# Optimization experiments

Hardware: AMD Instinct MI355X
Metric: run time of the kernel (lower is better)

Reference implementation:

```python
import jax, jax.numpy as jnp
import numpy as np

T_STEPS = 10       # T_pos = T_neg = 10 hardcoded in forward
ATTN_SCALE = 0.125 # scale hardcoded in forward (not head_dim**-0.5)
V_TH = 1.0         # spikingjelly IFNode defaults: v_threshold=1.0, v_reset=0.0 (hard reset)
SG_ALPHA = 4.0     # default Sigmoid surrogate alpha

@jax.custom_vjp
def spike(v):
    return (v >= 0.0).astype(v.dtype)

def _spike_fwd(v):
    return spike(v), v

def _spike_bwd(v, g):
    sg = jax.nn.sigmoid(SG_ALPHA * v)
    return (g * SG_ALPHA * sg * (1.0 - sg),)

spike.defvjp(_spike_fwd, _spike_bwd)

def if_node_const_input(y, T=T_STEPS):
    """Multi-step IF neuron driven by the SAME input y at every step.
    charge: v += y; fire: s = H(v - 1); hard reset: v = (1 - s) * v.
    Returns spikes of shape [T, *y.shape]."""
    def step(v, _):
        v = v + y
        s = spike(v - V_TH)
        v = (1.0 - s) * v
        return v, s
    _, spikes = jax.lax.scan(step, jnp.zeros_like(y), None, length=T)
    return spikes

def setup_inputs() -> dict:
    key = jax.random.key(0)
    ks = jax.random.split(key, 6)
    N, C = 2048, 2048
    x = jax.random.normal(ks[0], (N, C), dtype=jnp.float32)
    freqs_cis = jax.random.normal(ks[1], (N, 64), dtype=jnp.float32)  # unused by forward
    w_scale = 0.02
    wq = jax.random.normal(ks[2], (C, C), dtype=jnp.float32) * w_scale
    wk = jax.random.normal(ks[3], (C, C), dtype=jnp.float32) * w_scale
    wv = jax.random.normal(ks[4], (C, C), dtype=jnp.float32) * w_scale
    wo = jax.random.normal(ks[5], (C, C), dtype=jnp.float32) * w_scale
    return {"x": x, "freqs_cis": freqs_cis, "wq": wq, "wk": wk, "wv": wv, "wo": wo}

def reference(x, freqs_cis, wq, wk, wv, wo):
    N, C = x.shape
    n_heads, head_dim = 16, 128  # C == n_heads * head_dim; n_kv_heads == n_heads so repeat_kv is a no-op
    T = T_STEPS

    x_pos = jax.nn.relu(x)
    x_neg = jax.nn.relu(-x)

    # Input is identical at every timestep, so apply the linear once, then run IF over T.
    def branch(xb):
        q = if_node_const_input(xb @ wq)  # [T, N, C] binary spikes
        k = if_node_const_input(xb @ wk)
        v = if_node_const_input(xb @ wv)
        return q, k, v

    qp, kp, vp = branch(x_pos)
    qn, kn, vn = branch(x_neg)
    xq = (qp - qn).reshape(T, N, n_heads, head_dim)
    xk = (kp - kn).reshape(T, N, n_heads, head_dim)
    xv = (vp - vn).reshape(T, N, n_heads, head_dim)

    # no-softmax attention over the HEAD axis, per token: [T,N,H,H]
    attn = jnp.einsum('tnhd,tnmd->tnhm', xq, xk) * ATTN_SCALE
    x_attn = jnp.einsum('tnhm,tnmd->tnhd', attn, xv)          # [T,N,H,Dh]
    x_attn = jnp.swapaxes(x_attn, -1, -2).reshape(T, N, C)    # transpose(-1,-2) then merge

    xo = x_attn @ wo  # [T, N, C]
    return xo.mean(axis=0)
```

## Files before the change

kernel.cpp:

```cpp
#include <hip/hip_runtime.h>
#include <hip/hip_bf16.h>


#define LIST_CAP (512u * 1024u)
#define FLAG_EPS 4e-4f

typedef __attribute__((ext_vector_type(8))) short short8;
typedef __attribute__((ext_vector_type(16))) float floatx16;

__device__ const unsigned d_LUT[16] = {0u, 0x3FFu, 0x2AAu, 0x124u, 0x88u,
                                       0x210u, 0x20u, 0x40u, 0x80u, 0x100u,
                                       0x200u, 0u, 0u, 0u, 0u, 0u};

__device__ __forceinline__ void bf16x2_rne(float a, unsigned& p1, unsigned& p2) {
  const unsigned u = __float_as_uint(a);
  const unsigned t1 = u + 0x7FFFu + ((u >> 16) & 1u);
  p1 = t1 >> 16;
  const float r = a - __uint_as_float(t1 & 0xFFFF0000u);
  const unsigned u2 = __float_as_uint(r);
  p2 = (u2 + 0x7FFFu + ((u2 >> 16) & 1u)) >> 16;
}

template <int ZERO_CNT>
__global__ __launch_bounds__(256) void wsplit(
    const float* __restrict__ W0, const float* __restrict__ W1,
    const float* __restrict__ W2, unsigned short* __restrict__ Bpk,
    int NCT, unsigned* __restrict__ cnt) {
  if (ZERO_CNT && blockIdx.x == 0 && blockIdx.y == 0 && threadIdx.x == 0)
    *cnt = 0u;
  __shared__ float Wf[32 * 132];
  const int ct = blockIdx.x, k0 = blockIdx.y * 32;
  const int c0 = ct * 128;
  const int sel = c0 >> 11;
  const float* W = (sel == 0) ? W0 : ((sel == 1) ? W1 : W2);
  const int cc0 = c0 & 2047;
  const int t = threadIdx.x;

  const int kr = t >> 3, cq = (t & 7) * 16;
#pragma unroll
  for (int u = 0; u < 4; u++) {
    const float4 v = *(const float4*)(W + (size_t)(k0 + kr) * 2048 + cc0 + cq + 4 * u);
    *(float4*)&Wf[kr * 132 + cq + 4 * u] = v;
  }
  __syncthreads();

  const int cc = t >> 1, ch0 = (t & 1) * 2;
  unsigned short* img1 = Bpk + ((size_t)(0 * NCT + ct) * 64 + blockIdx.y) * 4096;
  unsigned short* img2 = Bpk + ((size_t)(1 * NCT + ct) * 64 + blockIdx.y) * 4096;
#pragma unroll
  for (int c = ch0; c < ch0 + 2; c++) {
    unsigned q1[8], q2[8];
#pragma unroll
    for (int e = 0; e < 8; e++) bf16x2_rne(Wf[(c * 8 + e) * 132 + cc], q1[e], q2[e]);
    const int off = cc * 32 + 8 * (c ^ ((cc >> 1) & 3));
    uint4 P1, P2;
    P1.x = q1[0] | (q1[1] << 16); P1.y = q1[2] | (q1[3] << 16);
    P1.z = q1[4] | (q1[5] << 16); P1.w = q1[6] | (q1[7] << 16);
    P2.x = q2[0] | (q2[1] << 16); P2.y = q2[2] | (q2[3] << 16);
    P2.z = q2[4] | (q2[5] << 16); P2.w = q2[6] | (q2[7] << 16);
    *(uint4*)&img1[off] = P1;
    *(uint4*)&img2[off] = P2;
  }
}

template <int RELU>
__global__ __launch_bounds__(256) void asplit(
    const float* __restrict__ src, unsigned short* __restrict__ Apk, int NRT) {
  const int rt = blockIdx.x, k0i = blockIdx.y;
  const int t = threadIdx.x;
  const int r = t >> 1, half = t & 1;
  int grow = rt * 128 + r;
  float sgn = 1.f;
  if (RELU && grow >= 2048) { grow -= 2048; sgn = -1.f; }
  const float* s = src + (size_t)grow * 2048 + k0i * 32 + half * 16;
  float f[16];
#pragma unroll
  for (int u = 0; u < 4; u++) {
    const float4 v = *(const float4*)(s + 4 * u);
    f[4 * u + 0] = v.x; f[4 * u + 1] = v.y;
    f[4 * u + 2] = v.z; f[4 * u + 3] = v.w;
  }
  if (RELU) {
#pragma unroll
    for (int e = 0; e < 16; e++) f[e] = fmaxf(sgn * f[e], 0.f);
  }
  unsigned q1[16], q2[16];
#pragma unroll
  for (int e = 0; e < 16; e++) bf16x2_rne(f[e], q1[e], q2[e]);

  unsigned short* img1 = Apk + ((size_t)(0 * NRT + rt) * 64 + k0i) * 4096;
  unsigned short* img2 = Apk + ((size_t)(1 * NRT + rt) * 64 + k0i) * 4096;
#pragma unroll
  for (int cc = 0; cc < 2; cc++) {
    const int c = half * 2 + cc;
    const int off = r * 32 + 8 * (c ^ ((r >> 1) & 3));
    const int e0 = cc * 8;
    uint4 P1, P2;
    P1.x = q1[e0 + 0] | (q1[e0 + 1] << 16); P1.y = q1[e0 + 2] | (q1[e0 + 3] << 16);
    P1.z = q1[e0 + 4] | (q1[e0 + 5] << 16); P1.w = q1[e0 + 6] | (q1[e0 + 7] << 16);
    P2.x = q2[e0 + 0] | (q2[e0 + 1] << 16); P2.y = q2[e0 + 2] | (q2[e0 + 3] << 16);
    P2.z = q2[e0 + 4] | (q2[e0 + 5] << 16); P2.w = q2[e0 + 6] | (q2[e0 + 7] << 16);
    *(uint4*)&img1[off] = P1;
    *(uint4*)&img2[off] = P2;
  }
}

template <int MODE>
__global__ __launch_bounds__(256, 4) void gemm_dma(
    const unsigned short* __restrict__ Apk, const unsigned short* __restrict__ Bpk,
    int NRT, int NCT, unsigned char* __restrict__ MaskJ,
    unsigned* __restrict__ list, unsigned* __restrict__ cnt,
    float* __restrict__ Out) {
  __shared__ unsigned short sh[4][4096];
  __shared__ unsigned lutS[16];

  const int tid = threadIdx.x;
  const int bx = blockIdx.x, by = blockIdx.y;
  const int lane = tid & 63, wave = tid >> 6;
  const int wr = wave >> 1, wc = wave & 1;
  const int lm = lane & 31, lg = lane >> 5;

  if (MODE == 0 && tid < 16) lutS[tid] = d_LUT[tid];

  const unsigned short* gsrc =
      (wave < 2) ? (Apk + ((size_t)(wave * NRT + by) * 64) * 4096)
                 : (Bpk + ((size_t)((wave - 2) * NCT + bx) * 64) * 4096);

  floatx16 acc[2][2];
#pragma unroll
  for (int i = 0; i < 2; i++)
#pragma unroll
    for (int j = 0; j < 2; j++)
#pragma unroll
      for (int e = 0; e < 16; e++) acc[i][j][e] = 0.f;

  for (int k0i = 0; k0i < 64; k0i++) {
    __syncthreads();
    const unsigned short* gp = gsrc + (size_t)k0i * 4096;
#pragma unroll
    for (int i = 0; i < 8; i++) {
      __builtin_amdgcn_global_load_lds(
          (const __attribute__((address_space(1))) unsigned*)(gp + i * 512 + lane * 8),
          (__attribute__((address_space(3))) unsigned*)(&sh[wave][i * 512]), 16, 0, 0);
    }
    __syncthreads();

#pragma unroll
    for (int ks = 0; ks < 2; ks++) {
      const int ch = ks * 2 + lg;
      short8 a1[2], a2[2], b1[2], b2[2];
#pragma unroll
      for (int it = 0; it < 2; it++) {
        const int row = 64 * wr + 32 * it + lm;
        const int off = row * 32 + 8 * (ch ^ ((row >> 1) & 3));
        a1[it] = *(const short8*)&sh[0][off];
        a2[it] = *(const short8*)&sh[1][off];
      }
#pragma unroll
      for (int jt = 0; jt < 2; jt++) {
        const int row = 64 * wc + 32 * jt + lm;
        const int off = row * 32 + 8 * (ch ^ ((row >> 1) & 3));
        b1[jt] = *(const short8*)&sh[2][off];
        b2[jt] = *(const short8*)&sh[3][off];
      }
#pragma unroll
      for (int it = 0; it < 2; it++)
#pragma unroll
        for (int jt = 0; jt < 2; jt++)
          acc[it][jt] = __builtin_amdgcn_mfma_f32_32x32x16_bf16(
              a1[it], b1[jt], acc[it][jt], 0, 0, 0);
#pragma unroll
      for (int it = 0; it < 2; it++)
#pragma unroll
        for (int jt = 0; jt < 2; jt++)
          acc[it][jt] = __builtin_amdgcn_mfma_f32_32x32x16_bf16(
              a1[it], b2[jt], acc[it][jt], 0, 0, 0);
#pragma unroll
      for (int it = 0; it < 2; it++)
#pragma unroll
        for (int jt = 0; jt < 2; jt++)
          acc[it][jt] = __builtin_amdgcn_mfma_f32_32x32x16_bf16(
              a2[it], b1[jt], acc[it][jt], 0, 0, 0);
    }
  }

#pragma unroll
  for (int it = 0; it < 2; it++) {
#pragma unroll
    for (int jt = 0; jt < 2; jt++) {
      const int gn = bx * 128 + 64 * wc + 32 * jt + lm;
#pragma unroll
      for (int reg = 0; reg < 16; reg++) {
        const int gm = by * 128 + 64 * wr + 32 * it + (reg & 3) + 8 * (reg >> 2) + 4 * lg;
        const float y = acc[it][jt][reg];
        if (MODE == 1) {
          Out[(size_t)gm * 2048 + gn] = y * 0.1f;
        } else {
          float r = __builtin_amdgcn_rcpf(y);
          r = fminf(fmaxf(r, -1.0f), 12.0f);
          const float jf = floorf(r);
          const float d0 = fmaf(jf, y, -1.0f);
          const float i0 = fminf(fmaxf(jf, 1.0f), 10.0f);
          const float i1 = fminf(fmaxf(jf + 1.0f, 1.0f), 10.0f);
          const float e0 = fmaf(i0, y, -1.0f);
          const float e1 = fmaf(i1, y, -1.0f);
          const float mind = fminf(fabsf(e0), fabsf(e1));
          const unsigned J = (unsigned)(int)((d0 >= 0.0f) ? jf : jf + 1.0f);
          MaskJ[(size_t)gm * 6144 + gn] = (unsigned char)((J <= 10u) ? J : 0u);
          if (mind < FLAG_EPS) {
            const unsigned idx = atomicAdd(cnt, 1u);
            if (idx < LIST_CAP) list[idx] = ((unsigned)gm << 13) | (unsigned)gn;
          }
        }
      }
    }
  }
}

__global__ __launch_bounds__(256) void transpose_w(
    const float* __restrict__ W0, const float* __restrict__ W1,
    const float* __restrict__ W2, float* __restrict__ WT) {
  __shared__ float tile[32][33];
  const int k0 = blockIdx.x * 32;
  const int c0 = blockIdx.y * 32;
  const int sel = c0 >> 11;
  const float* W = (sel == 0) ? W0 : ((sel == 1) ? W1 : W2);
  const int cc0 = c0 & 2047;
  const int tx = threadIdx.x, ty = threadIdx.y;
#pragma unroll
  for (int rep = 0; rep < 4; rep++)
    tile[ty + 8 * rep][tx] = W[(size_t)(k0 + ty + 8 * rep) * 2048 + cc0 + tx];
  __syncthreads();
#pragma unroll
  for (int rep = 0; rep < 4; rep++)
    WT[(size_t)(c0 + ty + 8 * rep) * 2048 + k0 + tx] = tile[tx][ty + 8 * rep];
}

__global__ __launch_bounds__(256) void rescue(
    const float* __restrict__ X, const float* __restrict__ WT,
    const unsigned* __restrict__ list, const unsigned* __restrict__ cnt,
    unsigned char* __restrict__ MaskJ) {
  const unsigned nItems = min(*cnt, LIST_CAP);
  const unsigned gtid = blockIdx.x * blockDim.x + threadIdx.x;
  const unsigned wave = gtid >> 6, lane = gtid & 63;
  const unsigned nWaves = (gridDim.x * blockDim.x) >> 6;

  for (unsigned i = wave; i < nItems; i += nWaves) {
    const unsigned e = list[i];
    const int r = (int)(e >> 13), c = (int)(e & 8191u);
    const float* xrow = X + (size_t)((r < 2048) ? r : r - 2048) * 2048;
    const float sg = (r < 2048) ? 1.f : -1.f;
    const float* wrow = WT + (size_t)c * 2048;
    double s = 0.0;
#pragma unroll
    for (int it = 0; it < 8; it++) {
      const int k = (it * 64 + (int)lane) * 4;
      const float4 xv = *(const float4*)(xrow + k);
      const float4 wv = *(const float4*)(wrow + k);
      const float a0 = fmaxf(sg * xv.x, 0.f);
      const float a1 = fmaxf(sg * xv.y, 0.f);
      const float a2 = fmaxf(sg * xv.z, 0.f);
      const float a3 = fmaxf(sg * xv.w, 0.f);
      s += (double)a0 * (double)wv.x + (double)a1 * (double)wv.y +
           (double)a2 * (double)wv.z + (double)a3 * (double)wv.w;
    }
#pragma unroll
    for (int off = 32; off > 0; off >>= 1) s += __shfl_down(s, off);
    if (lane == 0) {
      double v = 0.0;
      unsigned J = 0;
#pragma unroll
      for (int t = 0; t < 10; t++) {
        v += s;
        if (J == 0u && v >= 1.0) J = (unsigned)(t + 1);
      }
      MaskJ[(size_t)r * 6144 + c] = (unsigned char)J;
    }
  }
}

__global__ __launch_bounds__(256) void spike_attn(const unsigned char* __restrict__ MaskJ,
                                                  float* __restrict__ xbar) {
  const int n = blockIdx.x;
  const int tid = threadIdx.x;
  const int lane = tid & 63;

  __shared__ unsigned long long qpB[16][2], qnB[16][2], kpB[16][2], knB[16][2];
  __shared__ float xvT[16 * 132];
  __shared__ float attnS[16 * 17];
  __shared__ unsigned lutS[16];

  if (tid < 16) lutS[tid] = d_LUT[tid];
  __syncthreads();

  const unsigned char* mp = MaskJ + (size_t)n * 6144;
  const unsigned char* mn = MaskJ + (size_t)(n + 2048) * 6144;

  unsigned q_p[8], q_n[8], k_p[8], k_n[8], v_p[8], v_n[8];
#pragma unroll
  for (int j = 0; j < 8; j++) {
    const int c = tid + 256 * j;
    q_p[j] = lutS[mp[c]];        q_n[j] = lutS[mn[c]];
    k_p[j] = lutS[mp[2048 + c]]; k_n[j] = lutS[mn[2048 + c]];
    v_p[j] = lutS[mp[4096 + c]]; v_n[j] = lutS[mn[4096 + c]];
  }

  float acc[8];
#pragma unroll
  for (int j = 0; j < 8; j++) acc[j] = 0.f;

  for (int t = 0; t < 10; t++) {
#pragma unroll
    for (int j = 0; j < 8; j++) {
      const int c = tid + 256 * j;
      const unsigned long long bqp = __ballot((q_p[j] >> t) & 1u);
      const unsigned long long bqn = __ballot((q_n[j] >> t) & 1u);
      const unsigned long long bkp = __ballot((k_p[j] >> t) & 1u);
      const unsigned long long bkn = __ballot((k_n[j] >> t) & 1u);
      const int h = c >> 7, word = (c >> 6) & 1;
      if (lane == 0) {
        qpB[h][word] = bqp; qnB[h][word] = bqn;
        kpB[h][word] = bkp; knB[h][word] = bkn;
      }
      const int m = h, d = c & 127;
      xvT[m * 132 + d] =
          (float)((v_p[j] >> t) & 1u) - (float)((v_n[j] >> t) & 1u);
    }
    __syncthreads();

    {
      const int h = tid >> 4, m = tid & 15;
      int dot = 0;
#pragma unroll
      for (int w = 0; w < 2; w++) {
        const unsigned long long qp = qpB[h][w], qn = qnB[h][w];
        const unsigned long long kp = kpB[m][w], kn = knB[m][w];
        dot += __popcll(qp & kp) + __popcll(qn & kn) -
               __popcll(qp & kn) - __popcll(qn & kp);
      }
      attnS[h * 17 + m] = (float)dot * 0.125f;
    }
    __syncthreads();

    {
      const int h = tid & 15;
      float arow[16];
#pragma unroll
      for (int m = 0; m < 16; m++) arow[m] = attnS[h * 17 + m];
#pragma unroll
      for (int j = 0; j < 8; j++) {
        const int d = (tid + 256 * j) >> 4;
        float s = 0.f;
#pragma unroll
        for (int m = 0; m < 16; m++) s += arow[m] * xvT[m * 132 + d];
        acc[j] += s;
      }
    }
    __syncthreads();
  }

#pragma unroll
  for (int j = 0; j < 8; j++) xbar[(size_t)n * 2048 + tid + 256 * j] = acc[j];
}

extern "C" void kernel_launch(void* const* d_in, const int* in_sizes, int n_in,
                              void* d_out, int out_size, void* d_ws, size_t ws_size,
                              hipStream_t stream) {
  const float* x = (const float*)d_in[0];
  const float* wq = (const float*)d_in[2];
  const float* wk = (const float*)d_in[3];
  const float* wv = (const float*)d_in[4];
  const float* wo = (const float*)d_in[5];
  float* out = (float*)d_out;

  char* ws = (char*)d_ws;
  unsigned char* MaskJ = (unsigned char*)ws;
  unsigned short* WOpk = (unsigned short*)ws;
  char* reg2 = ws + (size_t)4096 * 6144;
  unsigned short* Bpk = (unsigned short*)reg2;
  float* WT = (float*)reg2;
  unsigned short* Xbpk = (unsigned short*)reg2;
  char* reg3 = reg2 + (size_t)6144 * 2048 * 2 * 2;
  unsigned short* Apk = (unsigned short*)reg3;
  float* xbar = (float*)reg3;
  unsigned* list = (unsigned*)(reg3 + (size_t)4096 * 2048 * 2 * 2);
  unsigned* cnt = list + LIST_CAP;

  wsplit<1><<<dim3(48, 64), 256, 0, stream>>>(wq, wk, wv, Bpk, 48, cnt);
  asplit<1><<<dim3(32, 64), 256, 0, stream>>>(x, Apk, 32);
  gemm_dma<0><<<dim3(48, 32), 256, 0, stream>>>(Apk, Bpk, 32, 48, MaskJ, list, cnt, nullptr);
  transpose_w<<<dim3(64, 192), dim3(32, 8), 0, stream>>>(wq, wk, wv, WT);
  rescue<<<2048, 256, 0, stream>>>(x, WT, list, cnt, MaskJ);
  spike_attn<<<2048, 256, 0, stream>>>(MaskJ, xbar);
  wsplit<0><<<dim3(16, 64), 256, 0, stream>>>(wo, wo, wo, WOpk, 16, nullptr);
  asplit<0><<<dim3(16, 64), 256, 0, stream>>>(xbar, Xbpk, 16);
  gemm_dma<1><<<dim3(16, 16), 256, 0, stream>>>(Xbpk, WOpk, 16, 16, nullptr, nullptr, nullptr, out);
}
```

Measured before the change: 803.4 us.

## Replace QKV projection GEMM with 256x256-tile double-buffered MFMA kernel

Adds a new gemm256 kernel for the large 4096x6144 QKV projection. It uses 256x256 output tiles with 8 waves, double-buffered LDS filled by global_load_lds, XCD-aware block remapping, and the 32x32x16 bf16 MFMA with setprio. The split kernels gain a FRAG layout that writes operands directly in MFMA fragment order, so LDS reads become contiguous per lane. The larger tiles raise data reuse and cut global traffic, at the cost of higher register and LDS pressure and only 384 workgroups.

```diff
diff --git a/kernel.cpp b/kernel.cpp
--- a/kernel.cpp
+++ b/kernel.cpp
@@ -21,7 +21,7 @@
   p2 = (u2 + 0x7FFFu + ((u2 >> 16) & 1u)) >> 16;
 }
 
-template <int ZERO_CNT>
+template <int ZERO_CNT, int FRAG>
 __global__ __launch_bounds__(256) void wsplit(
     const float* __restrict__ W0, const float* __restrict__ W1,
     const float* __restrict__ W2, unsigned short* __restrict__ Bpk,
@@ -45,25 +45,46 @@
   __syncthreads();
 
   const int cc = t >> 1, ch0 = (t & 1) * 2;
-  unsigned short* img1 = Bpk + ((size_t)(0 * NCT + ct) * 64 + blockIdx.y) * 4096;
-  unsigned short* img2 = Bpk + ((size_t)(1 * NCT + ct) * 64 + blockIdx.y) * 4096;
-#pragma unroll
-  for (int c = ch0; c < ch0 + 2; c++) {
-    unsigned q1[8], q2[8];
-#pragma unroll
-    for (int e = 0; e < 8; e++) bf16x2_rne(Wf[(c * 8 + e) * 132 + cc], q1[e], q2[e]);
-    const int off = cc * 32 + 8 * (c ^ ((cc >> 1) & 3));
-    uint4 P1, P2;
-    P1.x = q1[0] | (q1[1] << 16); P1.y = q1[2] | (q1[3] << 16);
-    P1.z = q1[4] | (q1[5] << 16); P1.w = q1[6] | (q1[7] << 16);
-    P2.x = q2[0] | (q2[1] << 16); P2.y = q2[2] | (q2[3] << 16);
-    P2.z = q2[4] | (q2[5] << 16); P2.w = q2[6] | (q2[7] << 16);
-    *(uint4*)&img1[off] = P1;
-    *(uint4*)&img2[off] = P2;
-  }
-}
-
-template <int RELU>
+  if (FRAG) {
+    unsigned short* base = Bpk + ((size_t)((ct >> 1) * 64 + blockIdx.y)) * 16384 +
+                           (size_t)(ct & 1) * 8192;
+#pragma unroll
+    for (int c = ch0; c < ch0 + 2; c++) {
+      unsigned q1[8], q2[8];
+#pragma unroll
+      for (int e = 0; e < 8; e++) bf16x2_rne(Wf[(c * 8 + e) * 132 + cc], q1[e], q2[e]);
+      const int ks = c >> 1, kh = c & 1;
+      const int off1 = ((0 * 2 + ks) * 4 + (cc >> 5)) * 512 + (kh * 32 + (cc & 31)) * 8;
+      const int off2 = ((1 * 2 + ks) * 4 + (cc >> 5)) * 512 + (kh * 32 + (cc & 31)) * 8;
+      uint4 P1, P2;
+      P1.x = q1[0] | (q1[1] << 16); P1.y = q1[2] | (q1[3] << 16);
+      P1.z = q1[4] | (q1[5] << 16); P1.w = q1[6] | (q1[7] << 16);
+      P2.x = q2[0] | (q2[1] << 16); P2.y = q2[2] | (q2[3] << 16);
+      P2.z = q2[4] | (q2[5] << 16); P2.w = q2[6] | (q2[7] << 16);
+      *(uint4*)&base[off1] = P1;
+      *(uint4*)&base[off2] = P2;
+    }
+  } else {
+    unsigned short* img1 = Bpk + ((size_t)(0 * NCT + ct) * 64 + blockIdx.y) * 4096;
+    unsigned short* img2 = Bpk + ((size_t)(1 * NCT + ct) * 64 + blockIdx.y) * 4096;
+#pragma unroll
+    for (int c = ch0; c < ch0 + 2; c++) {
+      unsigned q1[8], q2[8];
+#pragma unroll
+      for (int e = 0; e < 8; e++) bf16x2_rne(Wf[(c * 8 + e) * 132 + cc], q1[e], q2[e]);
+      const int off = cc * 32 + 8 * (c ^ ((cc >> 1) & 3));
+      uint4 P1, P2;
+      P1.x = q1[0] | (q1[1] << 16); P1.y = q1[2] | (q1[3] << 16);
+      P1.z = q1[4] | (q1[5] << 16); P1.w = q1[6] | (q1[7] << 16);
+      P2.x = q2[0] | (q2[1] << 16); P2.y = q2[2] | (q2[3] << 16);
+      P2.z = q2[4] | (q2[5] << 16); P2.w = q2[6] | (q2[7] << 16);
+      *(uint4*)&img1[off] = P1;
+      *(uint4*)&img2[off] = P2;
+    }
+  }
+}
+
+template <int RELU, int FRAG>
 __global__ __launch_bounds__(256) void asplit(
     const float* __restrict__ src, unsigned short* __restrict__ Apk, int NRT) {
   const int rt = blockIdx.x, k0i = blockIdx.y;
@@ -88,20 +109,154 @@
 #pragma unroll
   for (int e = 0; e < 16; e++) bf16x2_rne(f[e], q1[e], q2[e]);
 
-  unsigned short* img1 = Apk + ((size_t)(0 * NRT + rt) * 64 + k0i) * 4096;
-  unsigned short* img2 = Apk + ((size_t)(1 * NRT + rt) * 64 + k0i) * 4096;
-#pragma unroll
-  for (int cc = 0; cc < 2; cc++) {
-    const int c = half * 2 + cc;
-    const int off = r * 32 + 8 * (c ^ ((r >> 1) & 3));
-    const int e0 = cc * 8;
-    uint4 P1, P2;
-    P1.x = q1[e0 + 0] | (q1[e0 + 1] << 16); P1.y = q1[e0 + 2] | (q1[e0 + 3] << 16);
-    P1.z = q1[e0 + 4] | (q1[e0 + 5] << 16); P1.w = q1[e0 + 6] | (q1[e0 + 7] << 16);
-    P2.x = q2[e0 + 0] | (q2[e0 + 1] << 16); P2.y = q2[e0 + 2] | (q2[e0 + 3] << 16);
-    P2.z = q2[e0 + 4] | (q2[e0 + 5] << 16); P2.w = q2[e0 + 6] | (q2[e0 + 7] << 16);
-    *(uint4*)&img1[off] = P1;
-    *(uint4*)&img2[off] = P2;
+  if (FRAG) {
+    unsigned short* base = Apk + ((size_t)((rt >> 1) * 64 + k0i)) * 16384 +
+                           (size_t)(rt & 1) * 8192;
+#pragma unroll
+    for (int cc = 0; cc < 2; cc++) {
+      const int c = half * 2 + cc;
+      const int ks = c >> 1, kh = c & 1;
+      const int off1 = ((0 * 2 + ks) * 4 + (r >> 5)) * 512 + (kh * 32 + (r & 31)) * 8;
+      const int off2 = ((1 * 2 + ks) * 4 + (r >> 5)) * 512 + (kh * 32 + (r & 31)) * 8;
+      const int e0 = cc * 8;
+      uint4 P1, P2;
+      P1.x = q1[e0 + 0] | (q1[e0 + 1] << 16); P1.y = q1[e0 + 2] | (q1[e0 + 3] << 16);
+      P1.z = q1[e0 + 4] | (q1[e0 + 5] << 16); P1.w = q1[e0 + 6] | (q1[e0 + 7] << 16);
+      P2.x = q2[e0 + 0] | (q2[e0 + 1] << 16); P2.y = q2[e0 + 2] | (q2[e0 + 3] << 16);
+      P2.z = q2[e0 + 4] | (q2[e0 + 5] << 16); P2.w = q2[e0 + 6] | (q2[e0 + 7] << 16);
+      *(uint4*)&base[off1] = P1;
+      *(uint4*)&base[off2] = P2;
+    }
+  } else {
+    unsigned short* img1 = Apk + ((size_t)(0 * NRT + rt) * 64 + k0i) * 4096;
+    unsigned short* img2 = Apk + ((size_t)(1 * NRT + rt) * 64 + k0i) * 4096;
+#pragma unroll
+    for (int cc = 0; cc < 2; cc++) {
+      const int c = half * 2 + cc;
+      const int off = r * 32 + 8 * (c ^ ((r >> 1) & 3));
+      const int e0 = cc * 8;
+      uint4 P1, P2;
+      P1.x = q1[e0 + 0] | (q1[e0 + 1] << 16); P1.y = q1[e0 + 2] | (q1[e0 + 3] << 16);
+      P1.z = q1[e0 + 4] | (q1[e0 + 5] << 16); P1.w = q1[e0 + 6] | (q1[e0 + 7] << 16);
+      P2.x = q2[e0 + 0] | (q2[e0 + 1] << 16); P2.y = q2[e0 + 2] | (q2[e0 + 3] << 16);
+      P2.z = q2[e0 + 4] | (q2[e0 + 5] << 16); P2.w = q2[e0 + 6] | (q2[e0 + 7] << 16);
+      *(uint4*)&img1[off] = P1;
+      *(uint4*)&img2[off] = P2;
+    }
+  }
+}
+
+__global__ __launch_bounds__(512, 2) void gemm256(
+    const unsigned short* __restrict__ Apk, const unsigned short* __restrict__ Bpk,
+    unsigned char* __restrict__ MaskJ, unsigned* __restrict__ list,
+    unsigned* __restrict__ cnt) {
+  __shared__ unsigned short lds[2][4][8192];
+
+  const int tid = threadIdx.x;
+  const int wave = tid >> 6, lane = tid & 63;
+  const int lm = lane & 31, lg = lane >> 5;
+  const int wr = wave >> 2, wc = wave & 3;
+
+  const int orig = (int)blockIdx.x;
+  const int wg = (orig & 7) * 48 + (orig >> 3);
+  const int bx = wg % 24, by = wg / 24;
+
+  const unsigned short* Aimg = Apk + (size_t)by * 64 * 16384;
+  const unsigned short* Bimg = Bpk + (size_t)bx * 64 * 16384;
+
+  auto issue2 = [&](int kt, int nb, int c) {
+    const unsigned short* g = ((c < 2) ? (Aimg + (size_t)c * 8192)
+                                       : (Bimg + (size_t)(c - 2) * 8192)) +
+                              (size_t)kt * 16384;
+#pragma unroll
+    for (int rr = 0; rr < 2; rr++)
+      __builtin_amdgcn_global_load_lds(
+          (const __attribute__((address_space(1))) unsigned*)(g + rr * 4096 + tid * 8),
+          (__attribute__((address_space(3))) unsigned*)(&lds[nb][c][rr * 4096 + wave * 512]),
+          16, 0, 0);
+  };
+
+  floatx16 acc[4][2];
+#pragma unroll
+  for (int i = 0; i < 4; i++)
+#pragma unroll
+    for (int j = 0; j < 2; j++)
+#pragma unroll
+      for (int e = 0; e < 16; e++) acc[i][j][e] = 0.f;
+
+#pragma unroll
+  for (int c = 0; c < 4; c++) issue2(0, 0, c);
+  asm volatile("s_waitcnt vmcnt(0)" ::: "memory");
+  __builtin_amdgcn_s_barrier();
+  __builtin_amdgcn_sched_barrier(0);
+
+  const int rt0 = 2 * (wc & 1);
+  for (int kt = 0; kt < 64; kt++) {
+    const int cur = kt & 1, nxt = cur ^ 1;
+    const unsigned short* Ab = &lds[cur][wr][0];
+    const unsigned short* Bb = &lds[cur][2 + (wc >> 1)][0];
+#pragma unroll
+    for (int ks = 0; ks < 2; ks++) {
+      short8 a1[4], a2[4];
+#pragma unroll
+      for (int it = 0; it < 4; it++) {
+        a1[it] = *(const short8*)&Ab[((0 * 2 + ks) * 4 + it) * 512 + lane * 8];
+        a2[it] = *(const short8*)&Ab[((1 * 2 + ks) * 4 + it) * 512 + lane * 8];
+      }
+#pragma unroll
+      for (int jt = 0; jt < 2; jt++) {
+        const short8 b1 = *(const short8*)&Bb[((0 * 2 + ks) * 4 + rt0 + jt) * 512 + lane * 8];
+        const short8 b2 = *(const short8*)&Bb[((1 * 2 + ks) * 4 + rt0 + jt) * 512 + lane * 8];
+        if (ks == 0 && kt < 63) {
+          issue2(kt + 1, nxt, jt * 2 + 0);
+          issue2(kt + 1, nxt, jt * 2 + 1);
+        }
+        __builtin_amdgcn_s_barrier();
+        __builtin_amdgcn_s_setprio(1);
+#pragma unroll
+        for (int it = 0; it < 4; it++)
+          acc[it][jt] = __builtin_amdgcn_mfma_f32_32x32x16_bf16(a1[it], b1, acc[it][jt], 0, 0, 0);
+#pragma unroll
+        for (int it = 0; it < 4; it++)
+          acc[it][jt] = __builtin_amdgcn_mfma_f32_32x32x16_bf16(a1[it], b2, acc[it][jt], 0, 0, 0);
+#pragma unroll
+        for (int it = 0; it < 4; it++)
+          acc[it][jt] = __builtin_amdgcn_mfma_f32_32x32x16_bf16(a2[it], b1, acc[it][jt], 0, 0, 0);
+        __builtin_amdgcn_s_setprio(0);
+        if (ks == 1 && jt == 1)
+          asm volatile("s_waitcnt vmcnt(0)" ::: "memory");
+        __builtin_amdgcn_s_barrier();
+      }
+    }
+    __builtin_amdgcn_sched_barrier(0);
+  }
+
+#pragma unroll
+  for (int it = 0; it < 4; it++) {
+#pragma unroll
+    for (int jt = 0; jt < 2; jt++) {
+      const int gn = bx * 256 + 64 * wc + 32 * jt + lm;
+#pragma unroll
+      for (int reg = 0; reg < 16; reg++) {
+        const int gm = by * 256 + 128 * wr + 32 * it + (reg & 3) + 8 * (reg >> 2) + 4 * lg;
+        const float y = acc[it][jt][reg];
+        float r = __builtin_amdgcn_rcpf(y);
+        r = fminf(fmaxf(r, -1.0f), 12.0f);
+        const float jf = floorf(r);
+        const float d0 = fmaf(jf, y, -1.0f);
+        const float i0 = fminf(fmaxf(jf, 1.0f), 10.0f);
+        const float i1 = fminf(fmaxf(jf + 1.0f, 1.0f), 10.0f);
+        const float e0 = fmaf(i0, y, -1.0f);
+        const float e1 = fmaf(i1, y, -1.0f);
+        const float mind = fminf(fabsf(e0), fabsf(e1));
+        const unsigned J = (unsigned)(int)((d0 >= 0.0f) ? jf : jf + 1.0f);
+        MaskJ[(size_t)gm * 6144 + gn] = (unsigned char)((J <= 10u) ? J : 0u);
+        if (mind < FLAG_EPS) {
+          const unsigned idx = atomicAdd(cnt, 1u);
+          if (idx < LIST_CAP) list[idx] = ((unsigned)gm << 13) | (unsigned)gn;
+        }
+      }
+    }
   }
 }
 
@@ -112,15 +267,12 @@
     unsigned* __restrict__ list, unsigned* __restrict__ cnt,
     float* __restrict__ Out) {
   __shared__ unsigned short sh[4][4096];
-  __shared__ unsigned lutS[16];
 
   const int tid = threadIdx.x;
   const int bx = blockIdx.x, by = blockIdx.y;
   const int lane = tid & 63, wave = tid >> 6;
   const int wr = wave >> 1, wc = wave & 1;
   const int lm = lane & 31, lg = lane >> 5;
-
-  if (MODE == 0 && tid < 16) lutS[tid] = d_LUT[tid];
 
   const unsigned short* gsrc =
       (wave < 2) ? (Apk + ((size_t)(wave * NRT + by) * 64) * 4096)
@@ -386,13 +538,13 @@
   unsigned* list = (unsigned*)(reg3 + (size_t)4096 * 2048 * 2 * 2);
   unsigned* cnt = list + LIST_CAP;
 
-  wsplit<1><<<dim3(48, 64), 256, 0, stream>>>(wq, wk, wv, Bpk, 48, cnt);
-  asplit<1><<<dim3(32, 64), 256, 0, stream>>>(x, Apk, 32);
-  gemm_dma<0><<<dim3(48, 32), 256, 0, stream>>>(Apk, Bpk, 32, 48, MaskJ, list, cnt, nullptr);
+  wsplit<1, 1><<<dim3(48, 64), 256, 0, stream>>>(wq, wk, wv, Bpk, 48, cnt);
+  asplit<1, 1><<<dim3(32, 64), 256, 0, stream>>>(x, Apk, 32);
+  gemm256<<<384, 512, 0, stream>>>(Apk, Bpk, MaskJ, list, cnt);
   transpose_w<<<dim3(64, 192), dim3(32, 8), 0, stream>>>(wq, wk, wv, WT);
   rescue<<<2048, 256, 0, stream>>>(x, WT, list, cnt, MaskJ);
   spike_attn<<<2048, 256, 0, stream>>>(MaskJ, xbar);
-  wsplit<0><<<dim3(16, 64), 256, 0, stream>>>(wo, wo, wo, WOpk, 16, nullptr);
-  asplit<0><<<dim3(16, 64), 256, 0, stream>>>(xbar, Xbpk, 16);
+  wsplit<0, 0><<<dim3(16, 64), 256, 0, stream>>>(wo, wo, wo, WOpk, 16, nullptr);
+  asplit<0, 0><<<dim3(16, 64), 256, 0, stream>>>(xbar, Xbpk, 16);
   gemm_dma<1><<<dim3(16, 16), 256, 0, stream>>>(Xbpk, WOpk, 16, 16, nullptr, nullptr, nullptr, out);
 }
```

Measured after the change: 893.3 us. 1.11x slower.
